# Performance work log

Measured on AMD Instinct MI355X. Metric: run time of the kernel, lower is better.

The kernel has to match this reference:

```python
import jax, jax.numpy as jnp
import numpy as np

N, E, G = 65536, 524288, 1024
ND, ED, HID, H, C = 21, 12, 128, 4, 32
L = 8  # num_blocks * 2 conv layers
EPS = 1e-5


def _gatv2(x, src, dst, ea, Wl, Wr, We, att, bias):
    # PyG GATv2Conv: xl=lin_l(x) (source), xr=lin_r(x) (target)
    n = x.shape[0]
    xl = jnp.einsum('nd,dhc->nhc', x, Wl)   # [N,H,C]
    xr = jnp.einsum('nd,dhc->nhc', x, Wr)
    el = jnp.einsum('ed,dhc->ehc', ea, We)  # [E,H,C]
    m = xl[src] + xr[dst] + el              # per-edge message pre-activation
    e = jnp.einsum('ehc,hc->eh', jax.nn.leaky_relu(m, 0.2), att)  # [E,H]
    # scatter softmax over incoming edges of each dst node
    emax = jax.ops.segment_max(e, dst, num_segments=n)
    emax = jnp.where(jnp.isfinite(emax), emax, 0.0)
    p = jnp.exp(e - emax[dst])
    denom = jax.ops.segment_sum(p, dst, num_segments=n)
    alpha = p / jnp.clip(denom, 1e-16)[dst]
    out = jax.ops.segment_sum(alpha[..., None] * xl[src], dst, num_segments=n)
    return out.reshape(n, H * C) + bias


def _bn(x, scale, bias):
    mu = x.mean(0)
    var = x.var(0)
    return (x - mu) * jax.lax.rsqrt(var + EPS) * scale + bias


def setup_inputs():
    key = jax.random.key(0)
    ks = jax.random.split(key, 16)
    f = lambda k, shp, s=0.05: jax.random.normal(k, shp, jnp.float32) * s
    return dict(
        x=f(ks[0], (N, ND), 1.0),
        edge_attr=f(ks[1], (E, ED), 1.0),
        edge_index=jax.random.randint(ks[2], (2, E), 0, N),
        batch=jnp.sort(jax.random.randint(ks[3], (N,), 0, G)),
        Win=f(ks[4], (ND, HID)), bin_=jnp.zeros(HID),
        Wl=f(ks[5], (L, HID, H, C)), Wr=f(ks[6], (L, HID, H, C)),
        We=f(ks[7], (L, ED, H, C)), att=f(ks[8], (L, H, C)),
        bconv=jnp.zeros((L, HID)),
        bn_scale=jnp.ones((L, HID)), bn_bias=jnp.zeros((L, HID)),
        Wv1=f(ks[9], (HID, 64)), bv1=jnp.zeros(64),
        Wv2=f(ks[10], (64, 3)), bv2=jnp.zeros(3),
        Wp1=f(ks[11], (2 * HID + ED, 64)), bp1=jnp.zeros(64),
        Wp2=f(ks[12], (64, 1)), bp2=jnp.zeros(1),
    )


def reference(x, edge_attr, edge_index, batch, Win, bin_, Wl, Wr, We, att,
              bconv, bn_scale, bn_bias, Wv1, bv1, Wv2, bv2, Wp1, bp1, Wp2, bp2):
    src0, dst0 = edge_index[0], edge_index[1]
    # add_self_loops with fill_value='mean' for edge features
    ones_e = jnp.ones((E,), x.dtype)
    deg = jax.ops.segment_sum(ones_e, dst0, num_segments=N)
    mean_ea = jax.ops.segment_sum(edge_attr, dst0, num_segments=N) / jnp.clip(deg, 1.0)[:, None]
    ar = jnp.arange(N)
    src = jnp.concatenate([src0, ar])
    dst = jnp.concatenate([dst0, ar])
    ea = jnp.concatenate([edge_attr, mean_ea], axis=0)

    h = jax.nn.relu(x @ Win + bin_)
    for b in range(L // 2):
        i, j = 2 * b, 2 * b + 1
        res = h
        h = _gatv2(h, src, dst, ea, Wl[i], Wr[i], We[i], att[i], bconv[i])
        h = jax.nn.relu(_bn(h, bn_scale[i], bn_bias[i]))
        h = _gatv2(h, src, dst, ea, Wl[j], Wr[j], We[j], att[j], bconv[j])
        h = _bn(h, bn_scale[j], bn_bias[j])
        h = jax.nn.relu(h + res)

    counts = jax.ops.segment_sum(jnp.ones((N,), h.dtype), batch, num_segments=G)
    pooled = jax.ops.segment_sum(h, batch, num_segments=G) / jnp.clip(counts, 1.0)[:, None]
    value_logits = jax.nn.relu(pooled @ Wv1 + bv1) @ Wv2 + bv2  # [G,3]

    edge_input = jnp.concatenate([h[src0], h[dst0], edge_attr], axis=1)  # [E, 2*HID+ED]
    policy_logits = (jax.nn.relu(edge_input @ Wp1 + bp1) @ Wp2 + bp2)[:, 0]  # [E]
    return value_logits, policy_logits
```

## Files before the change

kernel.cpp:

```cpp
#include <hip/hip_runtime.h>
#include <hip/hip_fp16.h>

#define NN 65536
#define EE 524288
#define EPX 589824
#define GG 1024
#define NSLOT 32

typedef __attribute__((ext_vector_type(8))) short bf16x8;
typedef __attribute__((ext_vector_type(4))) float f32x4;

#define LOG2E 1.44269504088896f


__device__ __forceinline__ unsigned short f2bf(float x) {
    unsigned int u = __float_as_uint(x);
    u += 0x7FFFu + ((u >> 16) & 1u);
    return (unsigned short)(u >> 16);
}
__device__ __forceinline__ float bflo(unsigned int w) { return __uint_as_float(w << 16); }
__device__ __forceinline__ float bfhi(unsigned int w) { return __uint_as_float(w & 0xFFFF0000u); }
__device__ __forceinline__ float bf2f(unsigned short u) { return __uint_as_float((unsigned int)u << 16); }
__device__ __forceinline__ float lrelu(float x) { return fmaf(0.4f, fabsf(x), 0.6f * x); }
__device__ __forceinline__ unsigned int packh2(float a, float b) {
    __half2 h = __floats2half2_rn(a, b);
    return *reinterpret_cast<unsigned int*>(&h);
}
__device__ __forceinline__ unsigned long long rfl64(unsigned long long v) {
    unsigned int lo = __builtin_amdgcn_readfirstlane((unsigned int)v);
    unsigned int hi = __builtin_amdgcn_readfirstlane((unsigned int)(v >> 32));
    return (((unsigned long long)hi) << 32) | lo;
}

template <int CTRL>
__device__ __forceinline__ float dpp_add(float v) {
    int x = __builtin_amdgcn_update_dpp(0, __float_as_int(v), CTRL, 0xf, 0xf, true);
    return v + __int_as_float(x);
}
__device__ __forceinline__ float head_reduce(float t) {
    t = dpp_add<0xB1>(t);
    t = dpp_add<0x4E>(t);
    t = dpp_add<0x124>(t);
    t = dpp_add<0x128>(t);
    return t;
}


__launch_bounds__(256)
__global__ void k_deg(const int* __restrict__ dst0, int* __restrict__ deg)
{
    int e = blockIdx.x * 256 + threadIdx.x;
    if (e >= EE) return;
    atomicAdd(&deg[dst0[e]], 1);
}

__launch_bounds__(1024)
__global__ void k_scan(const int* __restrict__ deg, int* __restrict__ rowptr)
{
    __shared__ int sums[1024];
    int t = threadIdx.x;
    int base = t * 64;
    int s = 0;
    for (int i = 0; i < 64; i++) s += deg[base + i] + 1;
    sums[t] = s;
    __syncthreads();
    for (int off = 1; off < 1024; off <<= 1) {
        int v = (t >= off) ? sums[t - off] : 0;
        __syncthreads();
        sums[t] += v;
        __syncthreads();
    }
    int off = sums[t] - s;
    for (int i = 0; i < 64; i++) { rowptr[base + i] = off; off += deg[base + i] + 1; }
    if (t == 1023) rowptr[NN] = off;
}

__launch_bounds__(256)
__global__ void k_scatter(const int* __restrict__ src0, const int* __restrict__ dst0,
                          const float* __restrict__ eattr,
                          const int* __restrict__ rowptr, const int* __restrict__ deg,
                          int* __restrict__ fill, int* __restrict__ csr_src,
                          unsigned short* __restrict__ eaCSR)
{
    int e = blockIdx.x * 256 + threadIdx.x;
    if (e >= EPX) return;
    if (e < EE) {
        int d = dst0[e];
        int pos = rowptr[d] + atomicAdd(&fill[d], 1);
        csr_src[pos] = src0[e] << 8;
        const float* ep = eattr + (size_t)e * 12;
        float4 a = *reinterpret_cast<const float4*>(ep);
        float4 b = *reinterpret_cast<const float4*>(ep + 4);
        float4 c = *reinterpret_cast<const float4*>(ep + 8);
        unsigned short* o = eaCSR + (size_t)pos * 16;
        uint4 w; w.x = packh2(a.x, a.y); w.y = packh2(a.z, a.w);
        w.z = packh2(b.x, b.y); w.w = packh2(b.z, b.w);
        *reinterpret_cast<uint4*>(o) = w;
        *reinterpret_cast<uint2*>(o + 8) = make_uint2(packh2(c.x, c.y), packh2(c.z, c.w));
    } else {
        int n = e - EE;
        csr_src[rowptr[n] + deg[n]] = n << 8;
    }
}

__launch_bounds__(256)
__global__ void k_selfattr(const int* __restrict__ rowptr, unsigned short* __restrict__ eaCSR)
{
    int tid = blockIdx.x * 256 + threadIdx.x;
    int n = tid >> 4;
    int lk = tid & 15;
    if (lk >= 12) return;
    int beg = rowptr[n], endm1 = rowptr[n + 1] - 1;
    float s = 0.f;
    for (int p = beg; p < endm1; ++p) {
        __half h = *reinterpret_cast<const __half*>(&eaCSR[(size_t)p * 16 + lk]);
        s += __half2float(h);
    }
    float dv = fmaxf((float)(endm1 - beg), 1.0f);
    __half ho = __float2half(s / dv);
    eaCSR[(size_t)endm1 * 16 + lk] = *reinterpret_cast<unsigned short*>(&ho);
}


__launch_bounds__(256)
__global__ void k_wprep(const float* __restrict__ Wl, const float* __restrict__ Wr,
                        const float* __restrict__ Wp1,
                        unsigned short* __restrict__ wg, unsigned short* __restrict__ wp)
{
    int tid = blockIdx.x * 256 + threadIdx.x;
    if (tid < 32768) {
        int l = tid >> 12;
        int r = tid & 4095;
        int kt = r >> 10, ct = (r >> 6) & 15, lane = r & 63;
        int kb = kt * 32 + (lane >> 4) * 8;
        int col = ct * 16 + (lane & 15);
        const float* W = (col < 128) ? (Wl + (size_t)l * 16384 + col)
                                     : (Wr + (size_t)l * 16384 + (col - 128));
        unsigned short* o = wg + (size_t)tid * 8;
#pragma unroll
        for (int j = 0; j < 8; j++) o[j] = f2bf(W[(size_t)(kb + j) * 128]);
    } else if (tid < 34816) {
        int r = tid - 32768;
        int kt = r >> 9, ct = (r >> 6) & 7, lane = r & 63;
        int kb = kt * 32 + (lane >> 4) * 8;
        int col = ct * 16 + (lane & 15);
        const float* W = (col < 64) ? (Wp1 + col) : (Wp1 + 128 * 64 + (col - 64));
        unsigned short* o = wp + (size_t)r * 8;
#pragma unroll
        for (int j = 0; j < 8; j++) o[j] = f2bf(W[(size_t)(kb + j) * 64]);
    }
}


__launch_bounds__(256)
__global__ void k_input(const float* __restrict__ x, const float* __restrict__ Win,
                        const float* __restrict__ bin, float* __restrict__ h)
{
    __shared__ float W[21 * 128];
    int t = threadIdx.x;
    for (int i = t; i < 21 * 128; i += 256) W[i] = Win[i];
    __syncthreads();
    int c = t & 127, sub = t >> 7;
    int n0 = blockIdx.x * 16;
    float bc = bin[c];
    for (int i = 0; i < 8; i++) {
        int n = n0 + sub + i * 2;
        const float* xp = x + (size_t)n * 21;
        float acc = bc;
#pragma unroll
        for (int k = 0; k < 21; k++) acc = fmaf(xp[k], W[k * 128 + c], acc);
        h[(size_t)n * 128 + c] = fmaxf(acc, 0.f);
    }
}


__device__ __forceinline__ void load_afrag(const float* __restrict__ A, int arow, int kb,
                                           bf16x8 af[4])
{
#pragma unroll
    for (int kt = 0; kt < 4; kt++) {
        const float* ap = A + (size_t)arow * 128 + kt * 32 + kb;
        float4 lo = *reinterpret_cast<const float4*>(ap);
        float4 hi = *reinterpret_cast<const float4*>(ap + 4);
        bf16x8 v;
        v[0] = (short)f2bf(lo.x); v[1] = (short)f2bf(lo.y);
        v[2] = (short)f2bf(lo.z); v[3] = (short)f2bf(lo.w);
        v[4] = (short)f2bf(hi.x); v[5] = (short)f2bf(hi.y);
        v[6] = (short)f2bf(hi.z); v[7] = (short)f2bf(hi.w);
        af[kt] = v;
    }
}

__device__ __forceinline__ void gemm_gat_core(const bf16x8 af[4], const unsigned short* __restrict__ Bf,
                                              int row0, unsigned short* __restrict__ Cl,
                                              unsigned short* __restrict__ Cr, int lane)
{
    int crow = row0 + (lane >> 4) * 4;
    int c0 = lane & 15;
#pragma unroll
    for (int ct = 0; ct < 16; ct++) {
        f32x4 acc = {0.f, 0.f, 0.f, 0.f};
#pragma unroll
        for (int kt = 0; kt < 4; kt++) {
            bf16x8 bf = *reinterpret_cast<const bf16x8*>(Bf + ((size_t)(kt * 16 + ct) * 64 + lane) * 8);
            acc = __builtin_amdgcn_mfma_f32_16x16x32_bf16(af[kt], bf, acc, 0, 0, 0);
        }
        int col = ct * 16 + c0;
        unsigned short* C = (col < 128) ? Cl : Cr;
        int cc = col & 127;
#pragma unroll
        for (int r = 0; r < 4; r++)
            C[(size_t)(crow + r) * 128 + cc] = f2bf(acc[r]);
    }
}

__launch_bounds__(256)
__global__ void k_gemm_gat(const float* __restrict__ A, const unsigned short* __restrict__ Bf,
                           unsigned short* __restrict__ Cl, unsigned short* __restrict__ Cr)
{
    int wave = threadIdx.x >> 6, lane = threadIdx.x & 63;
    int row0 = blockIdx.x * 64 + wave * 16;
    bf16x8 af[4];
    load_afrag(A, row0 + (lane & 15), (lane >> 4) * 8, af);
    gemm_gat_core(af, Bf, row0, Cl, Cr, lane);
}

__launch_bounds__(256)
__global__ void k_gemm_gat_bn(const float* __restrict__ G, const float* __restrict__ bnstat,
                              const float* __restrict__ scale, const float* __restrict__ bias,
                              const unsigned short* __restrict__ Bf,
                              unsigned short* __restrict__ Cl, unsigned short* __restrict__ Cr)
{
    __shared__ float sA[128], bA[128];
    int t = threadIdx.x;
    if (t < 128) {
        float sum = 0.f, sq = 0.f;
#pragma unroll
        for (int sl = 0; sl < NSLOT; sl++) {
            sum += bnstat[sl * 256 + t];
            sq  += bnstat[sl * 256 + 128 + t];
        }
        const float invN = 1.0f / (float)NN;
        float mean = sum * invN;
        float var  = sq * invN - mean * mean;
        float sc   = scale[t] * rsqrtf(var + 1e-5f);
        sA[t] = sc;
        bA[t] = bias[t] - mean * sc;
    }
    __syncthreads();
    int wave = t >> 6, lane = t & 63;
    int row0 = blockIdx.x * 64 + wave * 16;
    int arow = row0 + (lane & 15);
    int kb = (lane >> 4) * 8;
    bf16x8 af[4];
#pragma unroll
    for (int kt = 0; kt < 4; kt++) {
        int cb = kt * 32 + kb;
        const float* gp = G + (size_t)arow * 128 + cb;
        float4 lo = *reinterpret_cast<const float4*>(gp);
        float4 hi = *reinterpret_cast<const float4*>(gp + 4);
        bf16x8 v;
        v[0] = (short)f2bf(fmaxf(fmaf(lo.x, sA[cb + 0], bA[cb + 0]), 0.f));
        v[1] = (short)f2bf(fmaxf(fmaf(lo.y, sA[cb + 1], bA[cb + 1]), 0.f));
        v[2] = (short)f2bf(fmaxf(fmaf(lo.z, sA[cb + 2], bA[cb + 2]), 0.f));
        v[3] = (short)f2bf(fmaxf(fmaf(lo.w, sA[cb + 3], bA[cb + 3]), 0.f));
        v[4] = (short)f2bf(fmaxf(fmaf(hi.x, sA[cb + 4], bA[cb + 4]), 0.f));
        v[5] = (short)f2bf(fmaxf(fmaf(hi.y, sA[cb + 5], bA[cb + 5]), 0.f));
        v[6] = (short)f2bf(fmaxf(fmaf(hi.z, sA[cb + 6], bA[cb + 6]), 0.f));
        v[7] = (short)f2bf(fmaxf(fmaf(hi.w, sA[cb + 7], bA[cb + 7]), 0.f));
        af[kt] = v;
    }
    gemm_gat_core(af, Bf, row0, Cl, Cr, lane);
}

__launch_bounds__(256)
__global__ void k_gemm_pol(const float* __restrict__ A, const unsigned short* __restrict__ Bf,
                           unsigned short* __restrict__ P)
{
    int wave = threadIdx.x >> 6, lane = threadIdx.x & 63;
    int row0 = blockIdx.x * 64 + wave * 16;
    bf16x8 af[4];
    load_afrag(A, row0 + (lane & 15), (lane >> 4) * 8, af);
    int crow = row0 + (lane >> 4) * 4;
    int c0 = lane & 15;
#pragma unroll
    for (int ct = 0; ct < 8; ct++) {
        f32x4 acc = {0.f, 0.f, 0.f, 0.f};
#pragma unroll
        for (int kt = 0; kt < 4; kt++) {
            bf16x8 bf = *reinterpret_cast<const bf16x8*>(Bf + ((size_t)(kt * 8 + ct) * 64 + lane) * 8);
            acc = __builtin_amdgcn_mfma_f32_16x16x32_bf16(af[kt], bf, acc, 0, 0, 0);
        }
        int col = ct * 16 + c0;
#pragma unroll
        for (int r = 0; r < 4; r++)
            P[(size_t)(crow + r) * 128 + col] = f2bf(acc[r]);
    }
}


__device__ __forceinline__ float2 edge_el(uint4 A, uint2 C,
                                          const __half2 wx[6], const __half2 wy[6])
{
    __half2 e0 = *reinterpret_cast<const __half2*>(&A.x);
    __half2 e1 = *reinterpret_cast<const __half2*>(&A.y);
    __half2 e2 = *reinterpret_cast<const __half2*>(&A.z);
    __half2 e3 = *reinterpret_cast<const __half2*>(&A.w);
    __half2 e4 = *reinterpret_cast<const __half2*>(&C.x);
    __half2 e5 = *reinterpret_cast<const __half2*>(&C.y);
    __half2 ax = __hmul2(e0, wx[0]);
    ax = __hfma2(e1, wx[1], ax); ax = __hfma2(e2, wx[2], ax);
    ax = __hfma2(e3, wx[3], ax); ax = __hfma2(e4, wx[4], ax);
    ax = __hfma2(e5, wx[5], ax);
    __half2 ay = __hmul2(e0, wy[0]);
    ay = __hfma2(e1, wy[1], ay); ay = __hfma2(e2, wy[2], ay);
    ay = __hfma2(e3, wy[3], ay); ay = __hfma2(e4, wy[4], ay);
    ay = __hfma2(e5, wy[5], ay);
    float2 r;
    r.x = __half2float(__hadd(__low2half(ax), __high2half(ax)));
    r.y = __half2float(__hadd(__low2half(ay), __high2half(ay)));
    return r;
}

__launch_bounds__(256)
__global__ void k_gat(const unsigned short* __restrict__ xlb, const unsigned short* __restrict__ xrb,
                      const unsigned short* __restrict__ eaCSR,
                      const int* __restrict__ rowptr, const int* __restrict__ csr_src,
                      const float* __restrict__ We, const float* __restrict__ att,
                      const float* __restrict__ bconv, float* __restrict__ g,
                      float* __restrict__ bnstat)
{
    int wid = blockIdx.x * 4 + (threadIdx.x >> 6);
    int lane = threadIdx.x & 63;
    int f0 = lane * 2;

    const int* cs_s = (const int*)rfl64((unsigned long long)csr_src);
    const unsigned short* ea_s = (const unsigned short*)rfl64((unsigned long long)eaCSR);

    __half2 wx[6], wy[6];
#pragma unroll
    for (int j = 0; j < 6; j++) {
        float2 w0 = *reinterpret_cast<const float2*>(We + (2 * j) * 128 + f0);
        float2 w1 = *reinterpret_cast<const float2*>(We + (2 * j + 1) * 128 + f0);
        wx[j] = __floats2half2_rn(w0.x, w1.x);
        wy[j] = __floats2half2_rn(w0.y, w1.y);
    }
    float2 av = *reinterpret_cast<const float2*>(att + f0);
    av.x *= LOG2E; av.y *= LOG2E;
    float2 bc = *reinterpret_cast<const float2*>(bconv + f0);
    const char* xl_lane = reinterpret_cast<const char*>(xlb) + (lane << 2);

    float bs0 = 0.f, bs1 = 0.f, bq0 = 0.f, bq1 = 0.f;

    for (int n = wid * 4; n < wid * 4 + 4; ++n) {
        unsigned int xrw = *reinterpret_cast<const unsigned int*>(xrb + (size_t)n * 128 + f0);
        float xr0 = bflo(xrw), xr1 = bfhi(xrw);

        float sA_ = 0.f, a0A = 0.f, a1A = 0.f;
        float sB_ = 0.f, a0B = 0.f, a1B = 0.f;
        int beg = rowptr[n], end = rowptr[n + 1];
        int idx = beg;
        for (; idx + 4 <= end; idx += 4) {
            int off0 = cs_s[idx],     off1 = cs_s[idx + 1];
            int off2 = cs_s[idx + 2], off3 = cs_s[idx + 3];
            const unsigned short* ep = ea_s + (size_t)idx * 16;
            uint4 qA = *reinterpret_cast<const uint4*>(ep);
            uint2 qC = *reinterpret_cast<const uint2*>(ep + 8);
            uint4 rA = *reinterpret_cast<const uint4*>(ep + 16);
            uint2 rC = *reinterpret_cast<const uint2*>(ep + 24);
            uint4 sAq = *reinterpret_cast<const uint4*>(ep + 32);
            uint2 sC = *reinterpret_cast<const uint2*>(ep + 40);
            uint4 tA = *reinterpret_cast<const uint4*>(ep + 48);
            uint2 tC = *reinterpret_cast<const uint2*>(ep + 56);
            unsigned int xw0 = *reinterpret_cast<const unsigned int*>(xl_lane + off0);
            unsigned int xw1 = *reinterpret_cast<const unsigned int*>(xl_lane + off1);
            unsigned int xw2 = *reinterpret_cast<const unsigned int*>(xl_lane + off2);
            unsigned int xw3 = *reinterpret_cast<const unsigned int*>(xl_lane + off3);

            float2 el0 = edge_el(qA, qC, wx, wy);
            float2 el1 = edge_el(rA, rC, wx, wy);
            float2 el2 = edge_el(sAq, sC, wx, wy);
            float2 el3 = edge_el(tA, tC, wx, wy);

            float xa0 = bflo(xw0), xa1 = bfhi(xw0);
            float xb0 = bflo(xw1), xb1 = bfhi(xw1);
            float xc0 = bflo(xw2), xc1 = bfhi(xw2);
            float xd0 = bflo(xw3), xd1 = bfhi(xw3);

            float t0 = lrelu(xa0 + xr0 + el0.x) * av.x + lrelu(xa1 + xr1 + el0.y) * av.y;
            float t1 = lrelu(xb0 + xr0 + el1.x) * av.x + lrelu(xb1 + xr1 + el1.y) * av.y;
            float t2 = lrelu(xc0 + xr0 + el2.x) * av.x + lrelu(xc1 + xr1 + el2.y) * av.y;
            float t3 = lrelu(xd0 + xr0 + el3.x) * av.x + lrelu(xd1 + xr1 + el3.y) * av.y;
            t0 = head_reduce(t0); t1 = head_reduce(t1);
            t2 = head_reduce(t2); t3 = head_reduce(t3);

            float w0 = exp2f(t0);
            float w1 = exp2f(t1);
            float w2 = exp2f(t2);
            float w3 = exp2f(t3);
            sA_ += w0 + w1;
            sB_ += w2 + w3;
            a0A = fmaf(w0, xa0, fmaf(w1, xb0, a0A));
            a1A = fmaf(w0, xa1, fmaf(w1, xb1, a1A));
            a0B = fmaf(w2, xc0, fmaf(w3, xd0, a0B));
            a1B = fmaf(w2, xc1, fmaf(w3, xd1, a1B));
        }
        for (; idx < end; ++idx) {
            int off0 = cs_s[idx];
            const unsigned short* ep = ea_s + (size_t)idx * 16;
            uint4 qA = *reinterpret_cast<const uint4*>(ep);
            uint2 qC = *reinterpret_cast<const uint2*>(ep + 8);
            unsigned int xw0 = *reinterpret_cast<const unsigned int*>(xl_lane + off0);
            float2 el0 = edge_el(qA, qC, wx, wy);
            float xa0 = bflo(xw0), xa1 = bfhi(xw0);
            float tt = lrelu(xa0 + xr0 + el0.x) * av.x + lrelu(xa1 + xr1 + el0.y) * av.y;
            tt = head_reduce(tt);
            float w = exp2f(tt);
            sA_ += w;
            a0A = fmaf(w, xa0, a0A);
            a1A = fmaf(w, xa1, a1A);
        }
        float s  = sA_ + sB_;
        float a0 = a0A + a0B;
        float a1 = a1A + a1B;
        float inv = 1.f / s;
        float r0 = fmaf(a0, inv, bc.x);
        float r1 = fmaf(a1, inv, bc.y);
        *reinterpret_cast<float2*>(g + (size_t)n * 128 + f0) = make_float2(r0, r1);
        bs0 += r0; bs1 += r1;
        bq0 = fmaf(r0, r0, bq0); bq1 = fmaf(r1, r1, bq1);
    }

    __shared__ float red[256 * 4];
    int t = threadIdx.x;
    red[t * 4 + 0] = bs0; red[t * 4 + 1] = bs1;
    red[t * 4 + 2] = bq0; red[t * 4 + 3] = bq1;
    __syncthreads();
    if (t < 64) {
        float v0 = red[t * 4 + 0] + red[(t + 64) * 4 + 0] + red[(t + 128) * 4 + 0] + red[(t + 192) * 4 + 0];
        float v1 = red[t * 4 + 1] + red[(t + 64) * 4 + 1] + red[(t + 128) * 4 + 1] + red[(t + 192) * 4 + 1];
        float q0 = red[t * 4 + 2] + red[(t + 64) * 4 + 2] + red[(t + 128) * 4 + 2] + red[(t + 192) * 4 + 2];
        float q1 = red[t * 4 + 3] + red[(t + 64) * 4 + 3] + red[(t + 128) * 4 + 3] + red[(t + 192) * 4 + 3];
        float* slot = bnstat + (size_t)(blockIdx.x & (NSLOT - 1)) * 256;
        atomicAdd(&slot[2 * t + 0], v0);
        atomicAdd(&slot[2 * t + 1], v1);
        atomicAdd(&slot[128 + 2 * t + 0], q0);
        atomicAdd(&slot[128 + 2 * t + 1], q1);
    }
}


__launch_bounds__(256)
__global__ void k_bnapply_res_relu(const float4* __restrict__ gin,
                                   const float* __restrict__ bnstat,
                                   const float* __restrict__ scale, const float* __restrict__ bias,
                                   float4* __restrict__ hbuf)
{
    __shared__ float sA[128], bA[128];
    int t = threadIdx.x;
    if (t < 128) {
        float sum = 0.f, sq = 0.f;
#pragma unroll
        for (int sl = 0; sl < NSLOT; sl++) {
            sum += bnstat[sl * 256 + t];
            sq  += bnstat[sl * 256 + 128 + t];
        }
        const float invN = 1.0f / (float)NN;
        float mean = sum * invN;
        float var  = sq * invN - mean * mean;
        float sc   = scale[t] * rsqrtf(var + 1e-5f);
        sA[t] = sc;
        bA[t] = bias[t] - mean * sc;
    }
    __syncthreads();
    int idx = blockIdx.x * 256 + t;
    int c4 = (idx & 31) * 4;
    float4 v = gin[idx];
    float4 hv = hbuf[idx];
    float4 r;
    r.x = fmaxf(fmaf(v.x, sA[c4 + 0], bA[c4 + 0]) + hv.x, 0.f);
    r.y = fmaxf(fmaf(v.y, sA[c4 + 1], bA[c4 + 1]) + hv.y, 0.f);
    r.z = fmaxf(fmaf(v.z, sA[c4 + 2], bA[c4 + 2]) + hv.z, 0.f);
    r.w = fmaxf(fmaf(v.w, sA[c4 + 3], bA[c4 + 3]) + hv.w, 0.f);
    hbuf[idx] = r;
}


__launch_bounds__(128)
__global__ void k_pool(const float* __restrict__ h, const int* __restrict__ batch,
                       float* __restrict__ pooled, float* __restrict__ cnt)
{
    int c = threadIdx.x;
    int r0 = blockIdx.x * 128;
    int cur = batch[r0];
    float acc = 0.f;
    float run = 0.f;
    for (int i = 0; i < 128; ++i) {
        int r = r0 + i;
        int b = batch[r];
        if (b != cur) {
            atomicAdd(&pooled[(size_t)cur * 128 + c], acc);
            if (c == 0) atomicAdd(&cnt[cur], run);
            acc = 0.f; run = 0.f; cur = b;
        }
        acc += h[(size_t)r * 128 + c];
        run += 1.f;
    }
    atomicAdd(&pooled[(size_t)cur * 128 + c], acc);
    if (c == 0) atomicAdd(&cnt[cur], run);
}

__launch_bounds__(64)
__global__ void k_value(const float* __restrict__ pooled, const float* __restrict__ cnt,
                        const float* __restrict__ Wv1, const float* __restrict__ bv1,
                        const float* __restrict__ Wv2, const float* __restrict__ bv2,
                        float* __restrict__ out)
{
    int gi = blockIdx.x;
    int l = threadIdx.x;
    float inv = 1.f / fmaxf(cnt[gi], 1.f);
    const float* pr = pooled + (size_t)gi * 128;
    float z = bv1[l];
    for (int k = 0; k < 128; k++) z = fmaf(pr[k] * inv, Wv1[k * 64 + l], z);
    z = fmaxf(z, 0.f);
#pragma unroll
    for (int j = 0; j < 3; j++) {
        float p = z * Wv2[l * 3 + j];
        p += __shfl_xor(p, 32); p += __shfl_xor(p, 16); p += __shfl_xor(p, 8);
        p += __shfl_xor(p, 4);  p += __shfl_xor(p, 2);  p += __shfl_xor(p, 1);
        if (l == 0) out[gi * 3 + j] = p + bv2[j];
    }
}


__launch_bounds__(256)
__global__ void k_policy(const unsigned short* __restrict__ P,
                         const float* __restrict__ eattr,
                         const int* __restrict__ src0, const int* __restrict__ dst0,
                         const float* __restrict__ Wp1c, const float* __restrict__ bp1,
                         const float* __restrict__ Wp2, const float* __restrict__ bp2,
                         float* __restrict__ out)
{
    int wave = (blockIdx.x * 256 + threadIdx.x) >> 6;
    int lane = threadIdx.x & 63;
    const float* ea_s = (const float*)rfl64((unsigned long long)eattr);
    const int* s_s = (const int*)rfl64((unsigned long long)src0);
    const int* d_s = (const int*)rfl64((unsigned long long)dst0);
    float w1c[12];
#pragma unroll
    for (int k = 0; k < 12; k++) w1c[k] = Wp1c[k * 64 + lane];
    float wp2 = Wp2[lane];
    float bb = bp1[lane];
    float b2 = bp2[0];
    for (int i = 0; i < 8; i += 2) {
        int e0i = wave * 8 + i;
        int e1i = e0i + 1;
        int sI0 = s_s[e0i], dI0 = d_s[e0i];
        int sI1 = s_s[e1i], dI1 = d_s[e1i];
        const float* ep0 = ea_s + (size_t)e0i * 12;
        const float* ep1 = ea_s + (size_t)e1i * 12;
        float4 a0 = *reinterpret_cast<const float4*>(ep0);
        float4 a1 = *reinterpret_cast<const float4*>(ep0 + 4);
        float4 a2 = *reinterpret_cast<const float4*>(ep0 + 8);
        float4 b0 = *reinterpret_cast<const float4*>(ep1);
        float4 b1 = *reinterpret_cast<const float4*>(ep1 + 4);
        float4 b2v = *reinterpret_cast<const float4*>(ep1 + 8);
        unsigned short ps0 = P[(size_t)sI0 * 128 + lane];
        unsigned short pd0 = P[(size_t)dI0 * 128 + 64 + lane];
        unsigned short ps1 = P[(size_t)sI1 * 128 + lane];
        unsigned short pd1 = P[(size_t)dI1 * 128 + 64 + lane];

        float z0 = bf2f(ps0) + bf2f(pd0) + bb;
        z0 += a0.x * w1c[0] + a0.y * w1c[1] + a0.z * w1c[2]  + a0.w * w1c[3]
            + a1.x * w1c[4] + a1.y * w1c[5] + a1.z * w1c[6]  + a1.w * w1c[7]
            + a2.x * w1c[8] + a2.y * w1c[9] + a2.z * w1c[10] + a2.w * w1c[11];
        float z1 = bf2f(ps1) + bf2f(pd1) + bb;
        z1 += b0.x * w1c[0] + b0.y * w1c[1] + b0.z * w1c[2]   + b0.w * w1c[3]
            + b1.x * w1c[4] + b1.y * w1c[5] + b1.z * w1c[6]   + b1.w * w1c[7]
            + b2v.x * w1c[8] + b2v.y * w1c[9] + b2v.z * w1c[10] + b2v.w * w1c[11];
        float p0 = fmaxf(z0, 0.f) * wp2;
        float p1 = fmaxf(z1, 0.f) * wp2;
        p0 = head_reduce(p0);
        p1 = head_reduce(p1);
        p0 += __shfl_xor(p0, 16); p1 += __shfl_xor(p1, 16);
        p0 += __shfl_xor(p0, 32); p1 += __shfl_xor(p1, 32);
        if (lane == 0) {
            out[3072 + e0i] = p0 + b2;
            out[3072 + e1i] = p1 + b2;
        }
    }
}


extern "C" void kernel_launch(void* const* d_in, const int* in_sizes, int n_in,
                              void* d_out, int out_size, void* d_ws, size_t ws_size,
                              hipStream_t stream)
{
    const float* x     = (const float*)d_in[0];
    const float* eattr = (const float*)d_in[1];
    const int*   eidx  = (const int*)d_in[2];
    const int*   batch = (const int*)d_in[3];
    const float* Win   = (const float*)d_in[4];
    const float* bin   = (const float*)d_in[5];
    const float* Wl    = (const float*)d_in[6];
    const float* Wr    = (const float*)d_in[7];
    const float* We    = (const float*)d_in[8];
    const float* att   = (const float*)d_in[9];
    const float* bconv = (const float*)d_in[10];
    const float* bnsc  = (const float*)d_in[11];
    const float* bnbi  = (const float*)d_in[12];
    const float* Wv1   = (const float*)d_in[13];
    const float* bv1   = (const float*)d_in[14];
    const float* Wv2   = (const float*)d_in[15];
    const float* bv2   = (const float*)d_in[16];
    const float* Wp1   = (const float*)d_in[17];
    const float* bp1   = (const float*)d_in[18];
    const float* Wp2   = (const float*)d_in[19];
    const float* bp2   = (const float*)d_in[20];
    float* out = (float*)d_out;

    const int* src0 = eidx;
    const int* dst0 = eidx + EE;

    const size_t NH = (size_t)NN * 128;
    float* ws = (float*)d_ws;
    float* h  = ws;
    float* g  = h + NH;
    unsigned short* xlb = (unsigned short*)(g + NH);
    unsigned short* xrb = xlb + NH;
    unsigned short* eaCSR = xrb + NH;
    int* rowptr = (int*)(eaCSR + (size_t)EPX * 16);
    int* csr_src = rowptr + (NN + 1);
    int* deg  = csr_src + EPX;
    int* fill = deg + NN;
    float* bnstat = (float*)(fill + NN);
    float* pooled = bnstat + 8 * NSLOT * 256;
    float* cnt    = pooled + (size_t)GG * 128;
    size_t zero_elems = (size_t)NN + NN + 8 * NSLOT * 256 + (size_t)GG * 128 + GG;
    unsigned short* wg = (unsigned short*)(cnt + GG);
    unsigned short* wp = wg + 8 * 32768;

    hipMemsetAsync(deg, 0, zero_elems * sizeof(float), stream);

    k_deg<<<EE / 256, 256, 0, stream>>>(dst0, deg);
    k_scan<<<1, 1024, 0, stream>>>(deg, rowptr);
    k_scatter<<<EPX / 256, 256, 0, stream>>>(src0, dst0, eattr, rowptr, deg, fill, csr_src, eaCSR);
    k_selfattr<<<(NN * 16) / 256, 256, 0, stream>>>(rowptr, eaCSR);
    k_wprep<<<136, 256, 0, stream>>>(Wl, Wr, Wp1, wg, wp);

    k_input<<<NN / 16, 256, 0, stream>>>(x, Win, bin, h);

    for (int l = 0; l < 8; l++) {
        float* bs = bnstat + (size_t)l * NSLOT * 256;
        if (l % 2 == 0) {
            k_gemm_gat<<<NN / 64, 256, 0, stream>>>(h, wg + (size_t)l * 32768, xlb, xrb);
        } else {
            float* bsp = bnstat + (size_t)(l - 1) * NSLOT * 256;
            k_gemm_gat_bn<<<NN / 64, 256, 0, stream>>>(g, bsp,
                                                       bnsc + (size_t)(l - 1) * 128,
                                                       bnbi + (size_t)(l - 1) * 128,
                                                       wg + (size_t)l * 32768, xlb, xrb);
        }
        k_gat<<<NN / 16, 256, 0, stream>>>(xlb, xrb, eaCSR, rowptr, csr_src,
                                           We + (size_t)l * 1536, att + (size_t)l * 128,
                                           bconv + (size_t)l * 128, g, bs);
        if (l % 2 == 1) {
            k_bnapply_res_relu<<<(NN * 128 / 4) / 256, 256, 0, stream>>>(
                (const float4*)g, bs, bnsc + (size_t)l * 128, bnbi + (size_t)l * 128,
                (float4*)h);
        }
    }

    k_pool<<<NN / 128, 128, 0, stream>>>(h, batch, pooled, cnt);
    k_value<<<GG, 64, 0, stream>>>(pooled, cnt, Wv1, bv1, Wv2, bv2, out);

    unsigned short* P = xlb;
    k_gemm_pol<<<NN / 64, 256, 0, stream>>>(h, wp, P);
    k_policy<<<NN / 4, 256, 0, stream>>>(P, eattr, src0, dst0,
                                         Wp1 + 256 * 64, bp1, Wp2, bp2, out);
}
```

Measured before the change: 1.094 ms.

## Iterate policy head in CSR order and halve nodes per GAT wave

```diff
diff --git a/kernel.cpp b/kernel.cpp
--- a/kernel.cpp
+++ b/kernel.cpp
@@ -5,7 +5,7 @@
 #define EE 524288
 #define EPX 589824
 #define GG 1024
-#define NSLOT 32
+#define NSLOT 64
 
 typedef __attribute__((ext_vector_type(8))) short bf16x8;
 typedef __attribute__((ext_vector_type(4))) float f32x4;
@@ -80,6 +80,7 @@
                           const float* __restrict__ eattr,
                           const int* __restrict__ rowptr, const int* __restrict__ deg,
                           int* __restrict__ fill, int* __restrict__ csr_src,
+                          int* __restrict__ csr_dst, int* __restrict__ csr_eid,
                           unsigned short* __restrict__ eaCSR)
 {
     int e = blockIdx.x * 256 + threadIdx.x;
@@ -88,6 +89,8 @@
         int d = dst0[e];
         int pos = rowptr[d] + atomicAdd(&fill[d], 1);
         csr_src[pos] = src0[e] << 8;
+        csr_dst[pos] = d << 8;
+        csr_eid[pos] = e;
         const float* ep = eattr + (size_t)e * 12;
         float4 a = *reinterpret_cast<const float4*>(ep);
         float4 b = *reinterpret_cast<const float4*>(ep + 4);
@@ -99,7 +102,10 @@
         *reinterpret_cast<uint2*>(o + 8) = make_uint2(packh2(c.x, c.y), packh2(c.z, c.w));
     } else {
         int n = e - EE;
-        csr_src[rowptr[n] + deg[n]] = n << 8;
+        int pos = rowptr[n] + deg[n];
+        csr_src[pos] = n << 8;
+        csr_dst[pos] = n << 8;
+        csr_eid[pos] = -1;
     }
 }
 
@@ -352,7 +358,7 @@
 
     float bs0 = 0.f, bs1 = 0.f, bq0 = 0.f, bq1 = 0.f;
 
-    for (int n = wid * 4; n < wid * 4 + 4; ++n) {
+    for (int n = wid * 2; n < wid * 2 + 2; ++n) {
         unsigned int xrw = *reinterpret_cast<const unsigned int*>(xrb + (size_t)n * 128 + f0);
         float xr0 = bflo(xrw), xr1 = bfhi(xrw);
 
@@ -533,60 +539,76 @@
 }
 
 
+__device__ __forceinline__ void dec12(uint4 A, uint2 C, float* o)
+{
+    __half2 h;
+    h = *reinterpret_cast<__half2*>(&A.x); o[0] = __low2float(h); o[1]  = __high2float(h);
+    h = *reinterpret_cast<__half2*>(&A.y); o[2] = __low2float(h); o[3]  = __high2float(h);
+    h = *reinterpret_cast<__half2*>(&A.z); o[4] = __low2float(h); o[5]  = __high2float(h);
+    h = *reinterpret_cast<__half2*>(&A.w); o[6] = __low2float(h); o[7]  = __high2float(h);
+    h = *reinterpret_cast<__half2*>(&C.x); o[8] = __low2float(h); o[9]  = __high2float(h);
+    h = *reinterpret_cast<__half2*>(&C.y); o[10] = __low2float(h); o[11] = __high2float(h);
+}
+
 __launch_bounds__(256)
 __global__ void k_policy(const unsigned short* __restrict__ P,
-                         const float* __restrict__ eattr,
-                         const int* __restrict__ src0, const int* __restrict__ dst0,
+                         const unsigned short* __restrict__ eaCSR,
+                         const int* __restrict__ csr_src, const int* __restrict__ csr_dst,
+                         const int* __restrict__ csr_eid,
                          const float* __restrict__ Wp1c, const float* __restrict__ bp1,
                          const float* __restrict__ Wp2, const float* __restrict__ bp2,
                          float* __restrict__ out)
 {
     int wave = (blockIdx.x * 256 + threadIdx.x) >> 6;
     int lane = threadIdx.x & 63;
-    const float* ea_s = (const float*)rfl64((unsigned long long)eattr);
-    const int* s_s = (const int*)rfl64((unsigned long long)src0);
-    const int* d_s = (const int*)rfl64((unsigned long long)dst0);
+    const unsigned short* ea_s = (const unsigned short*)rfl64((unsigned long long)eaCSR);
+    const int* cs_s = (const int*)rfl64((unsigned long long)csr_src);
+    const int* cd_s = (const int*)rfl64((unsigned long long)csr_dst);
+    const int* ce_s = (const int*)rfl64((unsigned long long)csr_eid);
+    const char* Pb = reinterpret_cast<const char*>(P);
     float w1c[12];
 #pragma unroll
     for (int k = 0; k < 12; k++) w1c[k] = Wp1c[k * 64 + lane];
     float wp2 = Wp2[lane];
     float bb = bp1[lane];
     float b2 = bp2[0];
+    int lb = lane * 2;
     for (int i = 0; i < 8; i += 2) {
-        int e0i = wave * 8 + i;
-        int e1i = e0i + 1;
-        int sI0 = s_s[e0i], dI0 = d_s[e0i];
-        int sI1 = s_s[e1i], dI1 = d_s[e1i];
-        const float* ep0 = ea_s + (size_t)e0i * 12;
-        const float* ep1 = ea_s + (size_t)e1i * 12;
-        float4 a0 = *reinterpret_cast<const float4*>(ep0);
-        float4 a1 = *reinterpret_cast<const float4*>(ep0 + 4);
-        float4 a2 = *reinterpret_cast<const float4*>(ep0 + 8);
-        float4 b0 = *reinterpret_cast<const float4*>(ep1);
-        float4 b1 = *reinterpret_cast<const float4*>(ep1 + 4);
-        float4 b2v = *reinterpret_cast<const float4*>(ep1 + 8);
-        unsigned short ps0 = P[(size_t)sI0 * 128 + lane];
-        unsigned short pd0 = P[(size_t)dI0 * 128 + 64 + lane];
-        unsigned short ps1 = P[(size_t)sI1 * 128 + lane];
-        unsigned short pd1 = P[(size_t)dI1 * 128 + 64 + lane];
+        int p0 = wave * 8 + i;
+        int p1 = p0 + 1;
+        int e0 = ce_s[p0], e1 = ce_s[p1];
+        int so0 = cs_s[p0], so1 = cs_s[p1];
+        int do0 = cd_s[p0], do1 = cd_s[p1];
+        const unsigned short* a0p = ea_s + (size_t)p0 * 16;
+        uint4 A0 = *reinterpret_cast<const uint4*>(a0p);
+        uint2 C0 = *reinterpret_cast<const uint2*>(a0p + 8);
+        uint4 A1 = *reinterpret_cast<const uint4*>(a0p + 16);
+        uint2 C1 = *reinterpret_cast<const uint2*>(a0p + 24);
+        unsigned short ps0 = *reinterpret_cast<const unsigned short*>(Pb + so0 + lb);
+        unsigned short pd0 = *reinterpret_cast<const unsigned short*>(Pb + do0 + 128 + lb);
+        unsigned short ps1 = *reinterpret_cast<const unsigned short*>(Pb + so1 + lb);
+        unsigned short pd1 = *reinterpret_cast<const unsigned short*>(Pb + do1 + 128 + lb);
+
+        float ea0[12], ea1[12];
+        dec12(A0, C0, ea0);
+        dec12(A1, C1, ea1);
 
         float z0 = bf2f(ps0) + bf2f(pd0) + bb;
-        z0 += a0.x * w1c[0] + a0.y * w1c[1] + a0.z * w1c[2]  + a0.w * w1c[3]
-            + a1.x * w1c[4] + a1.y * w1c[5] + a1.z * w1c[6]  + a1.w * w1c[7]
-            + a2.x * w1c[8] + a2.y * w1c[9] + a2.z * w1c[10] + a2.w * w1c[11];
         float z1 = bf2f(ps1) + bf2f(pd1) + bb;
-        z1 += b0.x * w1c[0] + b0.y * w1c[1] + b0.z * w1c[2]   + b0.w * w1c[3]
-            + b1.x * w1c[4] + b1.y * w1c[5] + b1.z * w1c[6]   + b1.w * w1c[7]
-            + b2v.x * w1c[8] + b2v.y * w1c[9] + b2v.z * w1c[10] + b2v.w * w1c[11];
-        float p0 = fmaxf(z0, 0.f) * wp2;
-        float p1 = fmaxf(z1, 0.f) * wp2;
-        p0 = head_reduce(p0);
-        p1 = head_reduce(p1);
-        p0 += __shfl_xor(p0, 16); p1 += __shfl_xor(p1, 16);
-        p0 += __shfl_xor(p0, 32); p1 += __shfl_xor(p1, 32);
+#pragma unroll
+        for (int k = 0; k < 12; k++) {
+            z0 = fmaf(ea0[k], w1c[k], z0);
+            z1 = fmaf(ea1[k], w1c[k], z1);
+        }
+        float p0v = fmaxf(z0, 0.f) * wp2;
+        float p1v = fmaxf(z1, 0.f) * wp2;
+        p0v = head_reduce(p0v);
+        p1v = head_reduce(p1v);
+        p0v += __shfl_xor(p0v, 16); p1v += __shfl_xor(p1v, 16);
+        p0v += __shfl_xor(p0v, 32); p1v += __shfl_xor(p1v, 32);
         if (lane == 0) {
-            out[3072 + e0i] = p0 + b2;
-            out[3072 + e1i] = p1 + b2;
+            if (e0 >= 0) out[3072 + e0] = p0v + b2;
+            if (e1 >= 0) out[3072 + e1] = p1v + b2;
         }
     }
 }
@@ -631,7 +653,9 @@
     unsigned short* eaCSR = xrb + NH;
     int* rowptr = (int*)(eaCSR + (size_t)EPX * 16);
     int* csr_src = rowptr + (NN + 1);
-    int* deg  = csr_src + EPX;
+    int* csr_dst = csr_src + EPX;
+    int* csr_eid = csr_dst + EPX;
+    int* deg  = csr_eid + EPX;
     int* fill = deg + NN;
     float* bnstat = (float*)(fill + NN);
     float* pooled = bnstat + 8 * NSLOT * 256;
@@ -644,7 +668,8 @@
 
     k_deg<<<EE / 256, 256, 0, stream>>>(dst0, deg);
     k_scan<<<1, 1024, 0, stream>>>(deg, rowptr);
-    k_scatter<<<EPX / 256, 256, 0, stream>>>(src0, dst0, eattr, rowptr, deg, fill, csr_src, eaCSR);
+    k_scatter<<<EPX / 256, 256, 0, stream>>>(src0, dst0, eattr, rowptr, deg, fill,
+                                             csr_src, csr_dst, csr_eid, eaCSR);
     k_selfattr<<<(NN * 16) / 256, 256, 0, stream>>>(rowptr, eaCSR);
     k_wprep<<<136, 256, 0, stream>>>(Wl, Wr, Wp1, wg, wp);
 
@@ -661,9 +686,9 @@
                                                        bnbi + (size_t)(l - 1) * 128,
                                                        wg + (size_t)l * 32768, xlb, xrb);
         }
-        k_gat<<<NN / 16, 256, 0, stream>>>(xlb, xrb, eaCSR, rowptr, csr_src,
-                                           We + (size_t)l * 1536, att + (size_t)l * 128,
-                                           bconv + (size_t)l * 128, g, bs);
+        k_gat<<<NN / 8, 256, 0, stream>>>(xlb, xrb, eaCSR, rowptr, csr_src,
+                                          We + (size_t)l * 1536, att + (size_t)l * 128,
+                                          bconv + (size_t)l * 128, g, bs);
         if (l % 2 == 1) {
             k_bnapply_res_relu<<<(NN * 128 / 4) / 256, 256, 0, stream>>>(
                 (const float4*)g, bs, bnsc + (size_t)l * 128, bnbi + (size_t)l * 128,
@@ -676,6 +701,6 @@
 
     unsigned short* P = xlb;
     k_gemm_pol<<<NN / 64, 256, 0, stream>>>(h, wp, P);
-    k_policy<<<NN / 4, 256, 0, stream>>>(P, eattr, src0, dst0,
-                                         Wp1 + 256 * 64, bp1, Wp2, bp2, out);
-}
+    k_policy<<<(EPX / 8) / 4, 256, 0, stream>>>(P, eaCSR, csr_src, csr_dst, csr_eid,
+                                                Wp1 + 256 * 64, bp1, Wp2, bp2, out);
+}
```

Result: slower. 1.169 ms (+6.8%).
